# Performance work log

Measured on AMD Instinct MI355X. Metric: run time of the kernel, lower is better.

## Reference

```python
import jax, jax.numpy as jnp
import numpy as np

N = 50000       # nodes
E = 800000      # edges
H = 128         # hidden_channels
L = 5           # num_layers
EIN = 16        # edge_in_channels
G = 512         # graphs in batch
NODE_VOCAB = 100
BN_EPS = 1e-5


def setup_inputs() -> dict:
    key = jax.random.key(0)
    ks = jax.random.split(key, 12)
    s = 0.1  # init scale
    return {
        "x": jax.random.randint(ks[0], (N,), 0, NODE_VOCAB, dtype=jnp.int32),
        "edge_index": jax.random.randint(ks[1], (2, E), 0, N, dtype=jnp.int32),
        "edge_attr": jax.random.normal(ks[2], (E, EIN), jnp.float32),
        "batch": jnp.sort(jax.random.randint(ks[3], (N,), 0, G, dtype=jnp.int32)),
        "node_emb": jax.random.normal(ks[4], (NODE_VOCAB, H), jnp.float32) * s,
        "edge_W": jax.random.normal(ks[5], (L, EIN, H), jnp.float32) * s,
        "edge_b": jnp.zeros((L, H), jnp.float32),
        "eps": jnp.zeros((L,), jnp.float32),
        "W1": jax.random.normal(ks[6], (L, H, 2 * H), jnp.float32) * s,
        "b1": jnp.zeros((L, 2 * H), jnp.float32),
        "g1": jnp.ones((L, 2 * H), jnp.float32),
        "be1": jnp.zeros((L, 2 * H), jnp.float32),
        "W2": jax.random.normal(ks[7], (L, 2 * H, H), jnp.float32) * s,
        "b2": jnp.zeros((L, H), jnp.float32),
        "bn_g": jnp.ones((L, H), jnp.float32),
        "bn_b": jnp.zeros((L, H), jnp.float32),
        "out_W": jax.random.normal(ks[8], (H, H), jnp.float32) * s,
        "out_b": jnp.zeros((H,), jnp.float32),
    }


def _bn(h, gamma, beta):
    # training-mode BatchNorm1d: batch statistics over the node axis
    m = h.mean(0)
    v = jnp.mean((h - m) ** 2, axis=0)
    return (h - m) * jax.lax.rsqrt(v + BN_EPS) * gamma + beta


def reference(x, edge_index, edge_attr, batch, node_emb, edge_W, edge_b, eps,
              W1, b1, g1, be1, W2, b2, bn_g, bn_b, out_W, out_b):
    h = node_emb[x]                                   # [N,H] node encoder
    src, dst = edge_index[0], edge_index[1]
    for i in range(L):
        # EGINConv: edge encode, gather->relu->scatter-add, GIN MLP
        e = edge_attr @ edge_W[i] + edge_b[i]         # [E,H]
        msg = jax.nn.relu(h[src] + e)                 # gather + relu
        agg = jax.ops.segment_sum(msg, dst, num_segments=N)  # scatter-add
        z = (1.0 + eps[i]) * h + agg
        z = jax.nn.relu(_bn(z @ W1[i] + b1[i], g1[i], be1[i]))  # mlp inner
        h = _bn(z @ W2[i] + b2[i], bn_g[i], bn_b[i])  # inter-layer BN
        if i < L - 1:
            h = jax.nn.relu(h)                        # dropout: eval (identity)
    # global_mean_pool
    sums = jax.ops.segment_sum(h, batch, num_segments=G)
    cnt = jax.ops.segment_sum(jnp.ones((N, 1), h.dtype), batch, num_segments=G)
    pooled = sums / jnp.maximum(cnt, 1.0)
    return pooled @ out_W + out_b                     # [G,H]
```

## Files before the change

kernel.cpp:

```cpp
#include <hip/hip_runtime.h>
#include <hip/hip_fp16.h>

#define N_NODES 50000
#define N_EDGES 800000
#define HD 128
#define NLAYERS 5
#define EINC 16
#define NG 512
#define BN_EPS 1e-5f

typedef _Float16 half8 __attribute__((ext_vector_type(8)));
typedef _Float16 half2v __attribute__((ext_vector_type(2)));
typedef float f32x4 __attribute__((ext_vector_type(4)));
typedef float f32x2 __attribute__((ext_vector_type(2)));

__device__ inline half2v h2bc(uint32_t u) { return __builtin_bit_cast(half2v, u); }

__global__ __launch_bounds__(256) void k_embed(const int* __restrict__ x,
                                               const float* __restrict__ emb,
                                               _Float16* __restrict__ h) {
  int i = blockIdx.x * 256 + threadIdx.x;
  if (i < N_NODES * 16) {
    int n = i >> 4, cv = i & 15;
    const float* src = &emb[(size_t)x[n] * HD + cv * 8];
    float4 a0 = *(const float4*)&src[0];
    float4 a1 = *(const float4*)&src[4];
    half8 p;
    p[0] = (_Float16)a0.x; p[1] = (_Float16)a0.y; p[2] = (_Float16)a0.z; p[3] = (_Float16)a0.w;
    p[4] = (_Float16)a1.x; p[5] = (_Float16)a1.y; p[6] = (_Float16)a1.z; p[7] = (_Float16)a1.w;
    *(half8*)&h[(size_t)n * HD + cv * 8] = p;
  }
}

__global__ __launch_bounds__(256) void k_hist(const int* __restrict__ ei,
                                              int* __restrict__ deg) {
  int e = blockIdx.x * 256 + threadIdx.x;
  if (e < N_EDGES) atomicAdd(&deg[ei[N_EDGES + e]], 1);
}

__global__ __launch_bounds__(256) void k_scan1(const int* __restrict__ deg,
                                               int* __restrict__ incl,
                                               int* __restrict__ bsum) {
  __shared__ int s[256];
  int i = blockIdx.x * 256 + threadIdx.x;
  int v = (i < N_NODES) ? deg[i] : 0;
  s[threadIdx.x] = v;
  __syncthreads();
  for (int d = 1; d < 256; d <<= 1) {
    int t = (threadIdx.x >= d) ? s[threadIdx.x - d] : 0;
    __syncthreads();
    s[threadIdx.x] += t;
    __syncthreads();
  }
  if (i < N_NODES) incl[i] = s[threadIdx.x];
  if (threadIdx.x == 255) bsum[blockIdx.x] = s[255];
}

__global__ void k_scan2(int* __restrict__ bsum, int nb) {
  __shared__ int s[256];
  int v = (threadIdx.x < nb) ? bsum[threadIdx.x] : 0;
  s[threadIdx.x] = v;
  __syncthreads();
  for (int d = 1; d < 256; d <<= 1) {
    int t = (threadIdx.x >= d) ? s[threadIdx.x - d] : 0;
    __syncthreads();
    s[threadIdx.x] += t;
    __syncthreads();
  }
  if (threadIdx.x < nb) bsum[threadIdx.x] = s[threadIdx.x];
}

__global__ __launch_bounds__(256) void k_scan3(const int* __restrict__ deg,
                                               const int* __restrict__ incl,
                                               const int* __restrict__ bsum,
                                               int* __restrict__ offs,
                                               int* __restrict__ cursor) {
  int i = blockIdx.x * 256 + threadIdx.x;
  if (i < N_NODES) {
    int base = (blockIdx.x > 0) ? bsum[blockIdx.x - 1] : 0;
    int start = base + incl[i] - deg[i];
    offs[i] = start;
    cursor[i] = start;
    if (i == N_NODES - 1) offs[N_NODES] = N_EDGES;
  }
}

__global__ __launch_bounds__(256) void k_scatter(const int* __restrict__ ei,
                                                 int* __restrict__ cursor,
                                                 int2* __restrict__ edata) {
  int e = blockIdx.x * 256 + threadIdx.x;
  if (e < N_EDGES) {
    int dst = ei[N_EDGES + e];
    int pos = atomicAdd(&cursor[dst], 1);
    edata[pos] = make_int2(ei[e], e);
  }
}

__global__ __launch_bounds__(256) void k_permea(const int2* __restrict__ edata,
                                                const float* __restrict__ ea,
                                                int* __restrict__ srcs,
                                                uint32_t* __restrict__ ea_dup) {
  int p = blockIdx.x * 256 + threadIdx.x;
  if (p < N_EDGES) {
    int2 d = edata[p];
    srcs[p] = d.x;
    const float* r = &ea[(size_t)d.y * EINC];
    uint32_t* o = &ea_dup[(size_t)p * EINC];
#pragma unroll
    for (int k = 0; k < EINC; ++k) {
      _Float16 v = (_Float16)r[k];
      half2v dv; dv[0] = v; dv[1] = v;
      o[k] = __builtin_bit_cast(uint32_t, dv);
    }
  }
}

__global__ __launch_bounds__(256) void k_cvtw(const float* __restrict__ W1,
                                              const float* __restrict__ W2,
                                              const float* __restrict__ eW,
                                              _Float16* __restrict__ w1t,
                                              _Float16* __restrict__ w2t,
                                              _Float16* __restrict__ eWh) {
  int i = blockIdx.x * 256 + threadIdx.x;
  if (i < 163840) {
    int l = i >> 15, r = i & 32767;
    int n = r >> 7, k = r & 127;
    w1t[i] = (_Float16)W1[(size_t)l * 32768 + k * 256 + n];
  } else if (i < 327680) {
    int j = i - 163840;
    int l = j >> 15, r = j & 32767;
    int n = r >> 8, k = r & 255;
    w2t[j] = (_Float16)W2[(size_t)l * 32768 + k * 128 + n];
  } else if (i < 337920) {
    int j = i - 327680;
    eWh[j] = (_Float16)eW[j];
  }
}

__global__ __launch_bounds__(256) void k_aggr(const int* __restrict__ offs,
                                              const int* __restrict__ srcs,
                                              const uint32_t* __restrict__ ea_dup,
                                              const _Float16* __restrict__ eWh,
                                              const float* __restrict__ eb,
                                              const float* __restrict__ epsA, int layer,
                                              const _Float16* __restrict__ hraw,
                                              const float* __restrict__ gsum2,
                                              const float* __restrict__ gsq2,
                                              const float* __restrict__ bng,
                                              const float* __restrict__ bnb,
                                              int fuse_bn,
                                              _Float16* __restrict__ z) {
  __shared__ float sP[2 * HD];
  const int w = threadIdx.x >> 6;
  const int lane = threadIdx.x & 63;
  const int nodeIdx = w >> 1, sub = w & 1;
  const int n = blockIdx.x * 2 + nodeIdx;
  const int c0 = lane * 2;

  half2v wph[EINC];
#pragma unroll
  for (int k = 0; k < EINC; ++k) wph[k] = *(const half2v*)&eWh[k * HD + c0];
  half2v ebh; ebh[0] = (_Float16)eb[c0]; ebh[1] = (_Float16)eb[c0 + 1];
  half2v hz; hz[0] = (_Float16)0.f; hz[1] = (_Float16)0.f;
  half2v sch = hz, shh = hz;
  if (fuse_bn) {
    const float invN = 1.0f / (float)N_NODES;
    float m0 = gsum2[c0] * invN, m1 = gsum2[c0 + 1] * invN;
    float v0 = fmaxf(gsq2[c0] * invN - m0 * m0, 0.0f);
    float v1 = fmaxf(gsq2[c0 + 1] * invN - m1 * m1, 0.0f);
    float s0 = bng[c0] * rsqrtf(v0 + BN_EPS);
    float s1 = bng[c0 + 1] * rsqrtf(v1 + BN_EPS);
    sch[0] = (_Float16)s0; sch[1] = (_Float16)s1;
    shh[0] = (_Float16)(bnb[c0] - m0 * s0);
    shh[1] = (_Float16)(bnb[c0 + 1] - m1 * s1);
  }
  const float epsv = 1.0f + epsA[layer];

  f32x2 acc = {0.f, 0.f};
  if (n < N_NODES) {
    int j0 = offs[n], j1 = offs[n + 1];
    int jm = j0 + ((j1 - j0 + 1) >> 1);
    int ja = sub ? jm : j0;
    int jb = sub ? j1 : jm;

    int jj = ja;
    for (; jj + 3 < jb; jj += 4) {
      int ju = __builtin_amdgcn_readfirstlane(jj);
      const int* sj = &srcs[ju];
      int s0 = sj[0], s1 = sj[1], s2 = sj[2], s3 = sj[3];
      const uint32_t* ra = &ea_dup[(size_t)ju * EINC];
      half2v g0 = *(const half2v*)&hraw[(size_t)s0 * HD + c0];
      half2v g1 = *(const half2v*)&hraw[(size_t)s1 * HD + c0];
      half2v g2 = *(const half2v*)&hraw[(size_t)s2 * HD + c0];
      half2v g3 = *(const half2v*)&hraw[(size_t)s3 * HD + c0];
      half2v e0 = ebh, e1 = ebh, e2 = ebh, e3 = ebh;
#pragma unroll
      for (int k = 0; k < EINC; ++k) {
        half2v w2 = wph[k];
        e0 = __builtin_elementwise_fma(h2bc(ra[k]), w2, e0);
        e1 = __builtin_elementwise_fma(h2bc(ra[EINC + k]), w2, e1);
        e2 = __builtin_elementwise_fma(h2bc(ra[2 * EINC + k]), w2, e2);
        e3 = __builtin_elementwise_fma(h2bc(ra[3 * EINC + k]), w2, e3);
      }
      if (fuse_bn) {
        g0 = __builtin_elementwise_max(__builtin_elementwise_fma(g0, sch, shh), hz);
        g1 = __builtin_elementwise_max(__builtin_elementwise_fma(g1, sch, shh), hz);
        g2 = __builtin_elementwise_max(__builtin_elementwise_fma(g2, sch, shh), hz);
        g3 = __builtin_elementwise_max(__builtin_elementwise_fma(g3, sch, shh), hz);
      }
      half2v m0 = __builtin_elementwise_max(g0 + e0, hz);
      half2v m1 = __builtin_elementwise_max(g1 + e1, hz);
      half2v m2 = __builtin_elementwise_max(g2 + e2, hz);
      half2v m3 = __builtin_elementwise_max(g3 + e3, hz);
      acc[0] += (float)m0[0]; acc[1] += (float)m0[1];
      acc[0] += (float)m1[0]; acc[1] += (float)m1[1];
      acc[0] += (float)m2[0]; acc[1] += (float)m2[1];
      acc[0] += (float)m3[0]; acc[1] += (float)m3[1];
    }
    for (; jj < jb; ++jj) {
      int ju = __builtin_amdgcn_readfirstlane(jj);
      int s0 = srcs[ju];
      const uint32_t* ra = &ea_dup[(size_t)ju * EINC];
      half2v g0 = *(const half2v*)&hraw[(size_t)s0 * HD + c0];
      half2v e0 = ebh;
#pragma unroll
      for (int k = 0; k < EINC; ++k)
        e0 = __builtin_elementwise_fma(h2bc(ra[k]), wph[k], e0);
      if (fuse_bn)
        g0 = __builtin_elementwise_max(__builtin_elementwise_fma(g0, sch, shh), hz);
      half2v m0 = __builtin_elementwise_max(g0 + e0, hz);
      acc[0] += (float)m0[0]; acc[1] += (float)m0[1];
    }

    if (!sub) {
      half2v hv = *(const half2v*)&hraw[(size_t)n * HD + c0];
      if (fuse_bn) hv = __builtin_elementwise_max(__builtin_elementwise_fma(hv, sch, shh), hz);
      acc[0] += epsv * (float)hv[0];
      acc[1] += epsv * (float)hv[1];
    } else {
      sP[nodeIdx * HD + c0] = acc[0];
      sP[nodeIdx * HD + c0 + 1] = acc[1];
    }
  }
  __syncthreads();
  if (n < N_NODES && !sub) {
    acc[0] += sP[nodeIdx * HD + c0];
    acc[1] += sP[nodeIdx * HD + c0 + 1];
    half2v oz; oz[0] = (_Float16)acc[0]; oz[1] = (_Float16)acc[1];
    *(half2v*)&z[(size_t)n * HD + c0] = oz;
  }
}

__global__ __launch_bounds__(256) void k_gemm1m(const _Float16* __restrict__ z,
                                                const _Float16* __restrict__ w1t,
                                                const float* __restrict__ bias,
                                                _Float16* __restrict__ y1h,
                                                float* __restrict__ gsum,
                                                float* __restrict__ gsq) {
  __shared__ char smemRaw[20480];
  _Float16* sA = (_Float16*)smemRaw;
  _Float16* sBT = (_Float16*)(smemRaw + 10240);
  float* sOut = (float*)smemRaw;
  __shared__ float ssum[128], ssq[128];
  const int tid = threadIdx.x;
  const int lane = tid & 63;
  const int wid = tid >> 6;
  const int wm = wid >> 1, wn = wid & 1;
  const int m0 = blockIdx.x * 128;
  const int n0 = blockIdx.y * 128;

  if (tid < 128) { ssum[tid] = 0.f; ssq[tid] = 0.f; }

  f32x4 acc[4][4];
  const f32x4 zz = {0.f, 0.f, 0.f, 0.f};
#pragma unroll
  for (int a = 0; a < 4; ++a)
#pragma unroll
    for (int b = 0; b < 4; ++b) acc[a][b] = zz;

  const int srow = tid >> 1;
  const int skh = (tid & 1) * 16;

  for (int k0 = 0; k0 < 128; k0 += 32) {
    {
      int n = m0 + srow;
      half8 p0, p1;
      if (n < N_NODES) {
        p0 = *(const half8*)&z[(size_t)n * 128 + k0 + skh];
        p1 = *(const half8*)&z[(size_t)n * 128 + k0 + skh + 8];
      } else {
#pragma unroll
        for (int j = 0; j < 8; ++j) { p0[j] = (_Float16)0.f; p1[j] = (_Float16)0.f; }
      }
      *(half8*)&sA[srow * 40 + skh] = p0;
      *(half8*)&sA[srow * 40 + skh + 8] = p1;
    }
    {
      half8 u0 = *(const half8*)&w1t[(size_t)(n0 + srow) * 128 + k0 + skh];
      half8 u1 = *(const half8*)&w1t[(size_t)(n0 + srow) * 128 + k0 + skh + 8];
      *(half8*)&sBT[srow * 40 + skh] = u0;
      *(half8*)&sBT[srow * 40 + skh + 8] = u1;
    }
    __syncthreads();
    half8 af[4], bf[4];
#pragma unroll
    for (int t = 0; t < 4; ++t) {
      af[t] = *(const half8*)&sA[(wm * 64 + t * 16 + (lane & 15)) * 40 + (lane >> 4) * 8];
      bf[t] = *(const half8*)&sBT[(wn * 64 + t * 16 + (lane & 15)) * 40 + (lane >> 4) * 8];
    }
#pragma unroll
    for (int tm = 0; tm < 4; ++tm)
#pragma unroll
      for (int tn = 0; tn < 4; ++tn)
        acc[tm][tn] = __builtin_amdgcn_mfma_f32_16x16x32_f16(af[tm], bf[tn], acc[tm][tn], 0, 0, 0);
    __syncthreads();
  }

  float bsv[4];
#pragma unroll
  for (int tn = 0; tn < 4; ++tn) bsv[tn] = bias[n0 + wn * 64 + tn * 16 + (lane & 15)];
  {
    float sacc[4] = {0.f, 0.f, 0.f, 0.f}, qacc[4] = {0.f, 0.f, 0.f, 0.f};
#pragma unroll
    for (int tm = 0; tm < 4; ++tm) {
      int nbase = m0 + wm * 64 + tm * 16 + (lane >> 4) * 4;
#pragma unroll
      for (int r = 0; r < 4; ++r) {
        if (nbase + r < N_NODES) {
#pragma unroll
          for (int tn = 0; tn < 4; ++tn) {
            float v = acc[tm][tn][r] + bsv[tn];
            sacc[tn] += v; qacc[tn] += v * v;
          }
        }
      }
    }
#pragma unroll
    for (int tn = 0; tn < 4; ++tn) {
      int c = wn * 64 + tn * 16 + (lane & 15);
      atomicAdd(&ssum[c], sacc[tn]);
      atomicAdd(&ssq[c], qacc[tn]);
    }
  }

  for (int c = 0; c < 4; ++c) {
    __syncthreads();
    if (wm == (c >> 1)) {
#pragma unroll
      for (int t2 = 0; t2 < 2; ++t2) {
        int tm = (c & 1) * 2 + t2;
#pragma unroll
        for (int tn = 0; tn < 4; ++tn)
#pragma unroll
          for (int r = 0; r < 4; ++r)
            sOut[(t2 * 16 + (lane >> 4) * 4 + r) * 132 + wn * 64 + tn * 16 + (lane & 15)] =
                acc[tm][tn][r] + bsv[tn];
      }
    }
    __syncthreads();
    int row = tid >> 3;
    int cb = (tid & 7) * 16;
    int gn = m0 + c * 32 + row;
    if (gn < N_NODES) {
      const float* rp = &sOut[row * 132 + cb];
      half8 o0, o1;
#pragma unroll
      for (int q = 0; q < 8; ++q) o0[q] = (_Float16)rp[q];
#pragma unroll
      for (int q = 0; q < 8; ++q) o1[q] = (_Float16)rp[8 + q];
      *(half8*)&y1h[(size_t)gn * 256 + n0 + cb] = o0;
      *(half8*)&y1h[(size_t)gn * 256 + n0 + cb + 8] = o1;
    }
  }
  __syncthreads();
  if (tid < 128) {
    unsafeAtomicAdd(&gsum[n0 + tid], ssum[tid]);
    unsafeAtomicAdd(&gsq[n0 + tid], ssq[tid]);
  }
}

__global__ __launch_bounds__(256) void k_gemm2m(const _Float16* __restrict__ y1h,
                                                const float* __restrict__ gsum1,
                                                const float* __restrict__ gsq1,
                                                const float* __restrict__ g1r,
                                                const float* __restrict__ be1r,
                                                const _Float16* __restrict__ w2t,
                                                const float* __restrict__ bias,
                                                _Float16* __restrict__ y2,
                                                float* __restrict__ gsum,
                                                float* __restrict__ gsq) {
  __shared__ char smemRaw[16896];
  _Float16* sA = (_Float16*)smemRaw;
  _Float16* sBT = (_Float16*)(smemRaw + 5120);
  float* sOut = (float*)smemRaw;
  __shared__ float ssc[256], ssh[256];
  __shared__ float ssum[128], ssq[128];
  const int tid = threadIdx.x;
  const int lane = tid & 63;
  const int wid = tid >> 6;
  const int wm = wid >> 1, wn = wid & 1;
  const int m0 = blockIdx.x * 64;

  {
    const float invN = 1.0f / (float)N_NODES;
    float m = gsum1[tid] * invN;
    float v = fmaxf(gsq1[tid] * invN - m * m, 0.0f);
    float s = g1r[tid] * rsqrtf(v + BN_EPS);
    ssc[tid] = s;
    ssh[tid] = be1r[tid] - m * s;
  }
  if (tid < 128) { ssum[tid] = 0.f; ssq[tid] = 0.f; }
  __syncthreads();

  f32x4 acc[2][4];
  const f32x4 zz = {0.f, 0.f, 0.f, 0.f};
#pragma unroll
  for (int a = 0; a < 2; ++a)
#pragma unroll
    for (int b = 0; b < 4; ++b) acc[a][b] = zz;

  const int arow = tid >> 2;
  const int akq = (tid & 3) * 8;
  const int brow = tid >> 1;
  const int bkh = (tid & 1) * 16;

  for (int k0 = 0; k0 < 256; k0 += 32) {
    {
      int n = m0 + arow;
      half8 p;
      if (n < N_NODES) {
        half8 yv = *(const half8*)&y1h[(size_t)n * 256 + k0 + akq];
#pragma unroll
        for (int j = 0; j < 8; ++j) {
          float v = fmaxf((float)yv[j] * ssc[k0 + akq + j] + ssh[k0 + akq + j], 0.f);
          p[j] = (_Float16)v;
        }
      } else {
#pragma unroll
        for (int j = 0; j < 8; ++j) p[j] = (_Float16)0.f;
      }
      *(half8*)&sA[arow * 40 + akq] = p;
    }
    {
      half8 u0 = *(const half8*)&w2t[(size_t)brow * 256 + k0 + bkh];
      half8 u1 = *(const half8*)&w2t[(size_t)brow * 256 + k0 + bkh + 8];
      *(half8*)&sBT[brow * 40 + bkh] = u0;
      *(half8*)&sBT[brow * 40 + bkh + 8] = u1;
    }
    __syncthreads();
    half8 af[2], bf[4];
#pragma unroll
    for (int t = 0; t < 2; ++t)
      af[t] = *(const half8*)&sA[(wm * 32 + t * 16 + (lane & 15)) * 40 + (lane >> 4) * 8];
#pragma unroll
    for (int t = 0; t < 4; ++t)
      bf[t] = *(const half8*)&sBT[(wn * 64 + t * 16 + (lane & 15)) * 40 + (lane >> 4) * 8];
#pragma unroll
    for (int tm = 0; tm < 2; ++tm)
#pragma unroll
      for (int tn = 0; tn < 4; ++tn)
        acc[tm][tn] = __builtin_amdgcn_mfma_f32_16x16x32_f16(af[tm], bf[tn], acc[tm][tn], 0, 0, 0);
    __syncthreads();
  }

  float bsv[4];
#pragma unroll
  for (int tn = 0; tn < 4; ++tn) bsv[tn] = bias[wn * 64 + tn * 16 + (lane & 15)];
  {
    float sacc[4] = {0.f, 0.f, 0.f, 0.f}, qacc[4] = {0.f, 0.f, 0.f, 0.f};
#pragma unroll
    for (int tm = 0; tm < 2; ++tm) {
      int nbase = m0 + wm * 32 + tm * 16 + (lane >> 4) * 4;
#pragma unroll
      for (int r = 0; r < 4; ++r) {
        if (nbase + r < N_NODES) {
#pragma unroll
          for (int tn = 0; tn < 4; ++tn) {
            float v = acc[tm][tn][r] + bsv[tn];
            sacc[tn] += v; qacc[tn] += v * v;
          }
        }
      }
    }
#pragma unroll
    for (int tn = 0; tn < 4; ++tn) {
      int c = wn * 64 + tn * 16 + (lane & 15);
      atomicAdd(&ssum[c], sacc[tn]);
      atomicAdd(&ssq[c], qacc[tn]);
    }
  }

  for (int c = 0; c < 2; ++c) {
    __syncthreads();
    if (wm == c) {
#pragma unroll
      for (int tm = 0; tm < 2; ++tm)
#pragma unroll
        for (int tn = 0; tn < 4; ++tn)
#pragma unroll
          for (int r = 0; r < 4; ++r)
            sOut[(tm * 16 + (lane >> 4) * 4 + r) * 132 + wn * 64 + tn * 16 + (lane & 15)] =
                acc[tm][tn][r] + bsv[tn];
    }
    __syncthreads();
    int row = tid >> 3;
    int cb = (tid & 7) * 16;
    int gn = m0 + c * 32 + row;
    if (gn < N_NODES) {
      const float* rp = &sOut[row * 132 + cb];
      half8 o0, o1;
#pragma unroll
      for (int q = 0; q < 8; ++q) o0[q] = (_Float16)rp[q];
#pragma unroll
      for (int q = 0; q < 8; ++q) o1[q] = (_Float16)rp[8 + q];
      *(half8*)&y2[(size_t)gn * 128 + cb] = o0;
      *(half8*)&y2[(size_t)gn * 128 + cb + 8] = o1;
    }
  }
  __syncthreads();
  if (tid < 128) {
    unsafeAtomicAdd(&gsum[tid], ssum[tid]);
    unsafeAtomicAdd(&gsq[tid], ssq[tid]);
  }
}

__global__ void k_goff(const int* __restrict__ batch, int* __restrict__ goff) {
  int g = blockIdx.x * blockDim.x + threadIdx.x;
  if (g <= NG) {
    if (g == NG) { goff[g] = N_NODES; return; }
    int lo = 0, hi = N_NODES;
    while (lo < hi) { int mid = (lo + hi) >> 1; if (batch[mid] < g) lo = mid + 1; else hi = mid; }
    goff[g] = lo;
  }
}

__global__ __launch_bounds__(256) void k_poolseg(const _Float16* __restrict__ y2raw,
                                                 const float* __restrict__ gsum2,
                                                 const float* __restrict__ gsq2,
                                                 const float* __restrict__ bng,
                                                 const float* __restrict__ bnb,
                                                 const int* __restrict__ goff,
                                                 float* __restrict__ pooled) {
  __shared__ float sred[256];
  int g = blockIdx.x;
  int c = threadIdx.x & 127;
  int half = threadIdx.x >> 7;
  int n0 = goff[g], n1 = goff[g + 1];
  float s = 0.f;
  for (int n = n0 + half; n < n1; n += 2) s += (float)y2raw[(size_t)n * HD + c];
  sred[threadIdx.x] = s;
  __syncthreads();
  if (threadIdx.x < 128) {
    const float invN = 1.0f / (float)N_NODES;
    float m = gsum2[threadIdx.x] * invN;
    float v = fmaxf(gsq2[threadIdx.x] * invN - m * m, 0.0f);
    float scv = bng[threadIdx.x] * rsqrtf(v + BN_EPS);
    float shv = bnb[threadIdx.x] - m * scv;
    float tot = sred[threadIdx.x] + sred[threadIdx.x + 128];
    float cntf = fmaxf((float)(n1 - n0), 1.0f);
    pooled[g * HD + threadIdx.x] = scv * (tot / cntf) + shv;
  }
}

__global__ __launch_bounds__(128) void k_final(const float* __restrict__ pooled,
                                               const float* __restrict__ oW,
                                               const float* __restrict__ ob,
                                               float* __restrict__ out) {
  __shared__ float sP[HD];
  int g = blockIdx.x;
  int c = threadIdx.x;
  sP[c] = pooled[g * HD + c];
  __syncthreads();
  float acc = ob[c];
#pragma unroll 8
  for (int k = 0; k < HD; ++k) acc += sP[k] * oW[k * HD + c];
  out[g * HD + c] = acc;
}

extern "C" void kernel_launch(void* const* d_in, const int* in_sizes, int n_in,
                              void* d_out, int out_size, void* d_ws, size_t ws_size,
                              hipStream_t stream) {
  const int* x = (const int*)d_in[0];
  const int* ei = (const int*)d_in[1];
  const float* ea = (const float*)d_in[2];
  const int* batch = (const int*)d_in[3];
  const float* emb = (const float*)d_in[4];
  const float* eW = (const float*)d_in[5];
  const float* eb = (const float*)d_in[6];
  const float* epsA = (const float*)d_in[7];
  const float* W1 = (const float*)d_in[8];
  const float* b1 = (const float*)d_in[9];
  const float* g1 = (const float*)d_in[10];
  const float* be1 = (const float*)d_in[11];
  const float* W2 = (const float*)d_in[12];
  const float* b2 = (const float*)d_in[13];
  const float* bng = (const float*)d_in[14];
  const float* bnb = (const float*)d_in[15];
  const float* oW = (const float*)d_in[16];
  const float* ob = (const float*)d_in[17];
  float* out = (float*)d_out;

  int* ip = (int*)d_ws;
  int* deg = ip;
  int* incl = deg + 50000;
  int* offs = incl + 50000;
  int* cursor = offs + 50001;
  int2* edata = (int2*)(cursor + 50000 + 1);
  int* srcs = (int*)(edata + 800000);
  int* bsum = srcs + 800000;
  int* goff = bsum + 200;
  float* fp = (float*)(ip + 2600716);
  _Float16* h = (_Float16*)fp;
  _Float16* zbuf = (_Float16*)(fp + 3200000);
  _Float16* y1h = (_Float16*)(fp + 6400000);
  uint32_t* ea_dup = (uint32_t*)(fp + 12800000);
  float* statsA = fp + 25600000;
  float* pooled = statsA + 3840;
  _Float16* w1t = (_Float16*)(pooled + 65536);
  _Float16* w2t = w1t + 163840;
  _Float16* eWh = w2t + 163840;

  const int edge_blocks = (N_EDGES + 255) / 256;
  const int node_blocks = (N_NODES + 255) / 256;

  k_embed<<<(N_NODES * 16 + 255) / 256, 256, 0, stream>>>(x, emb, h);

  hipMemsetAsync(deg, 0, 50000 * sizeof(int), stream);
  hipMemsetAsync(statsA, 0, 3840 * sizeof(float), stream);
  k_hist<<<edge_blocks, 256, 0, stream>>>(ei, deg);
  k_scan1<<<node_blocks, 256, 0, stream>>>(deg, incl, bsum);
  k_scan2<<<1, 256, 0, stream>>>(bsum, node_blocks);
  k_scan3<<<node_blocks, 256, 0, stream>>>(deg, incl, bsum, offs, cursor);
  k_scatter<<<edge_blocks, 256, 0, stream>>>(ei, cursor, edata);
  k_permea<<<edge_blocks, 256, 0, stream>>>(edata, ea, srcs, ea_dup);
  k_goff<<<3, 256, 0, stream>>>(batch, goff);
  k_cvtw<<<(337920 + 255) / 256, 256, 0, stream>>>(W1, W2, eW, w1t, w2t, eWh);

  for (int l = 0; l < NLAYERS; ++l) {
    float* st = statsA + (size_t)l * 768;
    float* st2 = st + 512;
    const float* pst2 = statsA + (size_t)(l - 1) * 768 + 512;
    k_aggr<<<(N_NODES + 1) / 2, 256, 0, stream>>>(offs, srcs, ea_dup,
                                                  eWh + (size_t)l * EINC * HD, eb + l * HD,
                                                  epsA, l, h,
                                                  (l > 0) ? pst2 : statsA, (l > 0) ? pst2 + 128 : statsA,
                                                  bng + (l > 0 ? (l - 1) : 0) * HD,
                                                  bnb + (l > 0 ? (l - 1) : 0) * HD,
                                                  (l > 0) ? 1 : 0, zbuf);
    k_gemm1m<<<dim3(391, 2), 256, 0, stream>>>(zbuf, w1t + (size_t)l * 32768,
                                               b1 + l * 256, y1h, st, st + 256);
    k_gemm2m<<<782, 256, 0, stream>>>(y1h, st, st + 256, g1 + l * 256, be1 + l * 256,
                                      w2t + (size_t)l * 32768, b2 + l * HD, h,
                                      st2, st2 + 128);
  }

  {
    const float* lst2 = statsA + (size_t)(NLAYERS - 1) * 768 + 512;
    k_poolseg<<<NG, 256, 0, stream>>>(h, lst2, lst2 + 128,
                                      bng + (NLAYERS - 1) * HD, bnb + (NLAYERS - 1) * HD,
                                      goff, pooled);
  }
  k_final<<<NG, 128, 0, stream>>>(pooled, oW, ob, out);
}
```

Before: 966.7 us.

## Compute edge encodings with MFMA per edge chunk in the aggregation kernel

The aggregation kernel now computes the edge linear encoding with 16x16x32 f16 MFMA tiles over chunks of 32 CSR edges. Results are staged in shared memory before the gather/relu/sum, replacing per-lane scalar half2 FMAs over duplicated edge attributes. The edge-attribute buffer shrinks to plain packed f16, halving its traffic, and the edge weights are transposed for the B fragments. The cost is extra __syncthreads per chunk, shared-memory round trips, and MFMA work that is wasted on the zero-padded K half and on partial chunks.

```diff
diff --git a/kernel.cpp b/kernel.cpp
--- a/kernel.cpp
+++ b/kernel.cpp
@@ -8,13 +8,12 @@
 #define EINC 16
 #define NG 512
 #define BN_EPS 1e-5f
+#define CHUNK 32
 
 typedef _Float16 half8 __attribute__((ext_vector_type(8)));
 typedef _Float16 half2v __attribute__((ext_vector_type(2)));
 typedef float f32x4 __attribute__((ext_vector_type(4)));
 typedef float f32x2 __attribute__((ext_vector_type(2)));
-
-__device__ inline half2v h2bc(uint32_t u) { return __builtin_bit_cast(half2v, u); }
 
 __global__ __launch_bounds__(256) void k_embed(const int* __restrict__ x,
                                                const float* __restrict__ emb,
@@ -99,19 +98,23 @@
 __global__ __launch_bounds__(256) void k_permea(const int2* __restrict__ edata,
                                                 const float* __restrict__ ea,
                                                 int* __restrict__ srcs,
-                                                uint32_t* __restrict__ ea_dup) {
+                                                _Float16* __restrict__ ea_h) {
   int p = blockIdx.x * 256 + threadIdx.x;
   if (p < N_EDGES) {
     int2 d = edata[p];
     srcs[p] = d.x;
     const float* r = &ea[(size_t)d.y * EINC];
-    uint32_t* o = &ea_dup[(size_t)p * EINC];
-#pragma unroll
-    for (int k = 0; k < EINC; ++k) {
-      _Float16 v = (_Float16)r[k];
-      half2v dv; dv[0] = v; dv[1] = v;
-      o[k] = __builtin_bit_cast(uint32_t, dv);
-    }
+    half8 o0, o1;
+#pragma unroll
+    for (int k = 0; k < 8; ++k) { o0[k] = (_Float16)r[k]; o1[k] = (_Float16)r[8 + k]; }
+    *(half8*)&ea_h[(size_t)p * EINC] = o0;
+    *(half8*)&ea_h[(size_t)p * EINC + 8] = o1;
+  } else if (p < N_EDGES + 64) {
+    half8 zz;
+#pragma unroll
+    for (int k = 0; k < 8; ++k) zz[k] = (_Float16)0.f;
+    *(half8*)&ea_h[(size_t)p * EINC] = zz;
+    *(half8*)&ea_h[(size_t)p * EINC + 8] = zz;
   }
 }
 
@@ -120,7 +123,7 @@
                                               const float* __restrict__ eW,
                                               _Float16* __restrict__ w1t,
                                               _Float16* __restrict__ w2t,
-                                              _Float16* __restrict__ eWh) {
+                                              _Float16* __restrict__ eWt) {
   int i = blockIdx.x * 256 + threadIdx.x;
   if (i < 163840) {
     int l = i >> 15, r = i & 32767;
@@ -133,14 +136,16 @@
     w2t[j] = (_Float16)W2[(size_t)l * 32768 + k * 128 + n];
   } else if (i < 337920) {
     int j = i - 327680;
-    eWh[j] = (_Float16)eW[j];
+    int l = j >> 11, r = j & 2047;
+    int n = r >> 4, k = r & 15;
+    eWt[j] = (_Float16)eW[(size_t)l * 2048 + k * 128 + n];
   }
 }
 
 __global__ __launch_bounds__(256) void k_aggr(const int* __restrict__ offs,
                                               const int* __restrict__ srcs,
-                                              const uint32_t* __restrict__ ea_dup,
-                                              const _Float16* __restrict__ eWh,
+                                              const _Float16* __restrict__ ea_h,
+                                              const _Float16* __restrict__ eWt,
                                               const float* __restrict__ eb,
                                               const float* __restrict__ epsA, int layer,
                                               const _Float16* __restrict__ hraw,
@@ -150,17 +155,34 @@
                                               const float* __restrict__ bnb,
                                               int fuse_bn,
                                               _Float16* __restrict__ z) {
+  __shared__ _Float16 sE[CHUNK * HD];
+  __shared__ int sSrc[CHUNK];
   __shared__ float sP[2 * HD];
-  const int w = threadIdx.x >> 6;
-  const int lane = threadIdx.x & 63;
+  const int tid = threadIdx.x;
+  const int w = tid >> 6;
+  const int lane = tid & 63;
   const int nodeIdx = w >> 1, sub = w & 1;
-  const int n = blockIdx.x * 2 + nodeIdx;
+  const int n0 = blockIdx.x * 2;
+  const int n = n0 + nodeIdx;
   const int c0 = lane * 2;
 
-  half2v wph[EINC];
-#pragma unroll
-  for (int k = 0; k < EINC; ++k) wph[k] = *(const half2v*)&eWh[k * HD + c0];
-  half2v ebh; ebh[0] = (_Float16)eb[c0]; ebh[1] = (_Float16)eb[c0 + 1];
+  const int chw = w * 32;
+  const int l15 = lane & 15;
+  const int lg = lane >> 4;
+  half8 hzero8;
+#pragma unroll
+  for (int q = 0; q < 8; ++q) hzero8[q] = (_Float16)0.f;
+  half8 bfrag[2];
+  f32x4 cinit[2];
+#pragma unroll
+  for (int ct = 0; ct < 2; ++ct) {
+    int col = chw + ct * 16 + l15;
+    bfrag[ct] = (lg < 2) ? *(const half8*)&eWt[(size_t)col * EINC + lg * 8] : hzero8;
+    float bv = eb[col];
+    f32x4 ci; ci[0] = bv; ci[1] = bv; ci[2] = bv; ci[3] = bv;
+    cinit[ct] = ci;
+  }
+
   half2v hz; hz[0] = (_Float16)0.f; hz[1] = (_Float16)0.f;
   half2v sch = hz, shh = hz;
   if (fuse_bn) {
@@ -176,76 +198,57 @@
   }
   const float epsv = 1.0f + epsA[layer];
 
+  const int jA = offs[n0];
+  const int jEnd = offs[n0 + 2];
+  const int myLo = offs[n];
+  const int myHi = offs[n + 1];
+
   f32x2 acc = {0.f, 0.f};
-  if (n < N_NODES) {
-    int j0 = offs[n], j1 = offs[n + 1];
-    int jm = j0 + ((j1 - j0 + 1) >> 1);
-    int ja = sub ? jm : j0;
-    int jb = sub ? j1 : jm;
-
-    int jj = ja;
-    for (; jj + 3 < jb; jj += 4) {
-      int ju = __builtin_amdgcn_readfirstlane(jj);
-      const int* sj = &srcs[ju];
-      int s0 = sj[0], s1 = sj[1], s2 = sj[2], s3 = sj[3];
-      const uint32_t* ra = &ea_dup[(size_t)ju * EINC];
-      half2v g0 = *(const half2v*)&hraw[(size_t)s0 * HD + c0];
-      half2v g1 = *(const half2v*)&hraw[(size_t)s1 * HD + c0];
-      half2v g2 = *(const half2v*)&hraw[(size_t)s2 * HD + c0];
-      half2v g3 = *(const half2v*)&hraw[(size_t)s3 * HD + c0];
-      half2v e0 = ebh, e1 = ebh, e2 = ebh, e3 = ebh;
-#pragma unroll
-      for (int k = 0; k < EINC; ++k) {
-        half2v w2 = wph[k];
-        e0 = __builtin_elementwise_fma(h2bc(ra[k]), w2, e0);
-        e1 = __builtin_elementwise_fma(h2bc(ra[EINC + k]), w2, e1);
-        e2 = __builtin_elementwise_fma(h2bc(ra[2 * EINC + k]), w2, e2);
-        e3 = __builtin_elementwise_fma(h2bc(ra[3 * EINC + k]), w2, e3);
+  for (int base = jA; base < jEnd; base += CHUNK) {
+    int cnt = jEnd - base; if (cnt > CHUNK) cnt = CHUNK;
+    __syncthreads();
+    if (tid < CHUNK) sSrc[tid] = (base + tid < jEnd) ? srcs[base + tid] : 0;
+    half8 afrag[2];
+#pragma unroll
+    for (int et = 0; et < 2; ++et) {
+      size_t row = (size_t)base + et * 16 + l15;
+      afrag[et] = (lg < 2) ? *(const half8*)&ea_h[row * EINC + lg * 8] : hzero8;
+    }
+#pragma unroll
+    for (int et = 0; et < 2; ++et)
+#pragma unroll
+      for (int ct = 0; ct < 2; ++ct) {
+        f32x4 D = __builtin_amdgcn_mfma_f32_16x16x32_f16(afrag[et], bfrag[ct], cinit[ct], 0, 0, 0);
+#pragma unroll
+        for (int r = 0; r < 4; ++r)
+          sE[(et * 16 + lg * 4 + r) * HD + chw + ct * 16 + l15] = (_Float16)D[r];
       }
-      if (fuse_bn) {
-        g0 = __builtin_elementwise_max(__builtin_elementwise_fma(g0, sch, shh), hz);
-        g1 = __builtin_elementwise_max(__builtin_elementwise_fma(g1, sch, shh), hz);
-        g2 = __builtin_elementwise_max(__builtin_elementwise_fma(g2, sch, shh), hz);
-        g3 = __builtin_elementwise_max(__builtin_elementwise_fma(g3, sch, shh), hz);
-      }
-      half2v m0 = __builtin_elementwise_max(g0 + e0, hz);
-      half2v m1 = __builtin_elementwise_max(g1 + e1, hz);
-      half2v m2 = __builtin_elementwise_max(g2 + e2, hz);
-      half2v m3 = __builtin_elementwise_max(g3 + e3, hz);
-      acc[0] += (float)m0[0]; acc[1] += (float)m0[1];
-      acc[0] += (float)m1[0]; acc[1] += (float)m1[1];
-      acc[0] += (float)m2[0]; acc[1] += (float)m2[1];
-      acc[0] += (float)m3[0]; acc[1] += (float)m3[1];
-    }
-    for (; jj < jb; ++jj) {
-      int ju = __builtin_amdgcn_readfirstlane(jj);
-      int s0 = srcs[ju];
-      const uint32_t* ra = &ea_dup[(size_t)ju * EINC];
-      half2v g0 = *(const half2v*)&hraw[(size_t)s0 * HD + c0];
-      half2v e0 = ebh;
-#pragma unroll
-      for (int k = 0; k < EINC; ++k)
-        e0 = __builtin_elementwise_fma(h2bc(ra[k]), wph[k], e0);
-      if (fuse_bn)
-        g0 = __builtin_elementwise_max(__builtin_elementwise_fma(g0, sch, shh), hz);
-      half2v m0 = __builtin_elementwise_max(g0 + e0, hz);
-      acc[0] += (float)m0[0]; acc[1] += (float)m0[1];
-    }
-
-    if (!sub) {
-      half2v hv = *(const half2v*)&hraw[(size_t)n * HD + c0];
+    __syncthreads();
+    int lo = myLo > base ? myLo : base;
+    int hi = myHi < base + cnt ? myHi : base + cnt;
+    for (int j = lo + sub; j < hi; j += 2) {
+      int jl = j - base;
+      half2v e2 = *(const half2v*)&sE[jl * HD + c0];
+      int src = sSrc[jl];
+      half2v hv = *(const half2v*)&hraw[(size_t)src * HD + c0];
       if (fuse_bn) hv = __builtin_elementwise_max(__builtin_elementwise_fma(hv, sch, shh), hz);
-      acc[0] += epsv * (float)hv[0];
-      acc[1] += epsv * (float)hv[1];
-    } else {
-      sP[nodeIdx * HD + c0] = acc[0];
-      sP[nodeIdx * HD + c0 + 1] = acc[1];
-    }
-  }
-  __syncthreads();
-  if (n < N_NODES && !sub) {
-    acc[0] += sP[nodeIdx * HD + c0];
-    acc[1] += sP[nodeIdx * HD + c0 + 1];
+      half2v m = __builtin_elementwise_max(hv + e2, hz);
+      acc[0] += (float)m[0];
+      acc[1] += (float)m[1];
+    }
+  }
+
+  __syncthreads();
+  if (sub) {
+    sP[nodeIdx * HD + c0] = acc[0];
+    sP[nodeIdx * HD + c0 + 1] = acc[1];
+  }
+  __syncthreads();
+  if (!sub) {
+    half2v hv = *(const half2v*)&hraw[(size_t)n * HD + c0];
+    if (fuse_bn) hv = __builtin_elementwise_max(__builtin_elementwise_fma(hv, sch, shh), hz);
+    acc[0] += epsv * (float)hv[0] + sP[nodeIdx * HD + c0];
+    acc[1] += epsv * (float)hv[1] + sP[nodeIdx * HD + c0 + 1];
     half2v oz; oz[0] = (_Float16)acc[0]; oz[1] = (_Float16)acc[1];
     *(half2v*)&z[(size_t)n * HD + c0] = oz;
   }
@@ -283,11 +286,11 @@
 
   for (int k0 = 0; k0 < 128; k0 += 32) {
     {
-      int n = m0 + srow;
+      int nn = m0 + srow;
       half8 p0, p1;
-      if (n < N_NODES) {
-        p0 = *(const half8*)&z[(size_t)n * 128 + k0 + skh];
-        p1 = *(const half8*)&z[(size_t)n * 128 + k0 + skh + 8];
+      if (nn < N_NODES) {
+        p0 = *(const half8*)&z[(size_t)nn * 128 + k0 + skh];
+        p1 = *(const half8*)&z[(size_t)nn * 128 + k0 + skh + 8];
       } else {
 #pragma unroll
         for (int j = 0; j < 8; ++j) { p0[j] = (_Float16)0.f; p1[j] = (_Float16)0.f; }
@@ -426,10 +429,10 @@
 
   for (int k0 = 0; k0 < 256; k0 += 32) {
     {
-      int n = m0 + arow;
+      int nn = m0 + arow;
       half8 p;
-      if (n < N_NODES) {
-        half8 yv = *(const half8*)&y1h[(size_t)n * 256 + k0 + akq];
+      if (nn < N_NODES) {
+        half8 yv = *(const half8*)&y1h[(size_t)nn * 256 + k0 + akq];
 #pragma unroll
         for (int j = 0; j < 8; ++j) {
           float v = fmaxf((float)yv[j] * ssc[k0 + akq + j] + ssh[k0 + akq + j], 0.f);
@@ -613,12 +616,12 @@
   _Float16* h = (_Float16*)fp;
   _Float16* zbuf = (_Float16*)(fp + 3200000);
   _Float16* y1h = (_Float16*)(fp + 6400000);
-  uint32_t* ea_dup = (uint32_t*)(fp + 12800000);
-  float* statsA = fp + 25600000;
+  _Float16* ea_h = (_Float16*)(fp + 12800000);
+  float* statsA = fp + 19200512;
   float* pooled = statsA + 3840;
   _Float16* w1t = (_Float16*)(pooled + 65536);
   _Float16* w2t = w1t + 163840;
-  _Float16* eWh = w2t + 163840;
+  _Float16* eWt = w2t + 163840;
 
   const int edge_blocks = (N_EDGES + 255) / 256;
   const int node_blocks = (N_NODES + 255) / 256;
@@ -632,21 +635,21 @@
   k_scan2<<<1, 256, 0, stream>>>(bsum, node_blocks);
   k_scan3<<<node_blocks, 256, 0, stream>>>(deg, incl, bsum, offs, cursor);
   k_scatter<<<edge_blocks, 256, 0, stream>>>(ei, cursor, edata);
-  k_permea<<<edge_blocks, 256, 0, stream>>>(edata, ea, srcs, ea_dup);
+  k_permea<<<(N_EDGES + 64 + 255) / 256, 256, 0, stream>>>(edata, ea, srcs, ea_h);
   k_goff<<<3, 256, 0, stream>>>(batch, goff);
-  k_cvtw<<<(337920 + 255) / 256, 256, 0, stream>>>(W1, W2, eW, w1t, w2t, eWh);
+  k_cvtw<<<(337920 + 255) / 256, 256, 0, stream>>>(W1, W2, eW, w1t, w2t, eWt);
 
   for (int l = 0; l < NLAYERS; ++l) {
     float* st = statsA + (size_t)l * 768;
     float* st2 = st + 512;
     const float* pst2 = statsA + (size_t)(l - 1) * 768 + 512;
-    k_aggr<<<(N_NODES + 1) / 2, 256, 0, stream>>>(offs, srcs, ea_dup,
-                                                  eWh + (size_t)l * EINC * HD, eb + l * HD,
-                                                  epsA, l, h,
-                                                  (l > 0) ? pst2 : statsA, (l > 0) ? pst2 + 128 : statsA,
-                                                  bng + (l > 0 ? (l - 1) : 0) * HD,
-                                                  bnb + (l > 0 ? (l - 1) : 0) * HD,
-                                                  (l > 0) ? 1 : 0, zbuf);
+    k_aggr<<<N_NODES / 2, 256, 0, stream>>>(offs, srcs, ea_h,
+                                            eWt + (size_t)l * 2048, eb + l * HD,
+                                            epsA, l, h,
+                                            (l > 0) ? pst2 : statsA, (l > 0) ? pst2 + 128 : statsA,
+                                            bng + (l > 0 ? (l - 1) : 0) * HD,
+                                            bnb + (l > 0 ? (l - 1) : 0) * HD,
+                                            (l > 0) ? 1 : 0, zbuf);
     k_gemm1m<<<dim3(391, 2), 256, 0, stream>>>(zbuf, w1t + (size_t)l * 32768,
                                                b1 + l * 256, y1h, st, st + 256);
     k_gemm2m<<<782, 256, 0, stream>>>(y1h, st, st + 256, g1 + l * 256, be1 + l * 256,
```

Result: slower. 1.064 ms (+10.1%).
